# Kernel tuning notes

Hardware: AMD Instinct MI355X
Metric: run time of the kernel (lower is better)

## Reference

```python
import jax, jax.numpy as jnp
import numpy as np

B, L, HID, H, D = 1, 2048, 3072, 24, 128
MLP = 4 * HID
LH, LW = 32, 56      # latent mask grid -> LH*LW image tokens at the END of the sequence
LIP = 16             # IP-adapter image tokens
IP_SCALE = 0.6


def setup_inputs() -> dict:
    key = jax.random.key(0)
    k = jax.random.split(key, 10)
    # Flux rotary pe layout [1,1,L,D//2,2,2]: pe[...,0]=[cos,-sin], pe[...,1]=[sin,cos]
    pos = jnp.arange(L, dtype=jnp.float32)
    freqs = 1.0 / (10000.0 ** (jnp.arange(0, D, 2, dtype=jnp.float32) / D))
    ang = pos[:, None] * freqs[None, :]            # [L, D//2]
    cos, sin = jnp.cos(ang), jnp.sin(ang)
    pe = jnp.stack([jnp.stack([cos, -sin], -1), jnp.stack([sin, cos], -1)], -2)[None, None]
    return {
        "x": jax.random.normal(k[0], (B, L, HID), jnp.float32),
        "vec": jax.random.normal(k[1], (B, HID), jnp.float32),
        "pe": pe,
        "img_mask": jax.random.uniform(k[2], (B, LH, LW), jnp.float32),
        "image_emb": jax.random.normal(k[3], (B, LIP, HID), jnp.float32),
        "mod_w": jax.random.normal(k[4], (3 * HID, HID), jnp.float32) * 0.02,
        "mod_b": jnp.zeros((3 * HID,), jnp.float32),
        "lin1_w": jax.random.normal(k[5], (3 * HID + MLP, HID), jnp.float32) * 0.02,
        "lin1_b": jnp.zeros((3 * HID + MLP,), jnp.float32),
        "q_scale": jnp.ones((D,), jnp.float32),
        "k_scale": jnp.ones((D,), jnp.float32),
        "lin2_w": jax.random.normal(k[6], (HID, HID + MLP), jnp.float32) * 0.02,
        "lin2_b": jnp.zeros((HID,), jnp.float32),
        "ipk_w": jax.random.normal(k[7], (HID, HID), jnp.float32) * 0.02,
        "ipv_w": jax.random.normal(k[8], (HID, HID), jnp.float32) * 0.02,
    }


def _rms(x, scale, eps):
    # RMSNorm over last dim (QKNorm / norm_added_k)
    return x * jax.lax.rsqrt(jnp.mean(x * x, -1, keepdims=True) + eps) * scale


def _apply_rope(x, pe):
    # x: [B,H,L,D]; pe: [1,1,L,D//2,2,2]
    xr = x.reshape(x.shape[:-1] + (D // 2, 1, 2))
    out = pe[..., 0] * xr[..., 0] + pe[..., 1] * xr[..., 1]  # [B,H,L,D//2,2]
    return out.reshape(x.shape)


def _sdpa(q, k, v):
    # q:[B,H,Lq,D] k,v:[B,H,Lk,D] -> [B,Lq,H*D]
    s = jnp.einsum('bhqd,bhkd->bhqk', q, k) / jnp.sqrt(jnp.float32(D))
    o = jnp.einsum('bhqk,bhkd->bhqd', jax.nn.softmax(s, -1), v)
    return o.transpose(0, 2, 1, 3).reshape(q.shape[0], q.shape[2], H * D)


def reference(x, vec, pe, img_mask, image_emb, mod_w, mod_b, lin1_w, lin1_b,
              q_scale, k_scale, lin2_w, lin2_b, ipk_w, ipv_w):
    # modulation: SiLU(vec) -> Linear -> (shift, scale, gate), each [B,1,HID]
    mod = jax.nn.silu(vec) @ mod_w.T + mod_b
    shift, scale, gate = [m[:, None, :] for m in jnp.split(mod, 3, -1)]
    # pre_norm: LayerNorm, no affine, eps 1e-6 (biased variance, matches torch)
    ln = (x - jnp.mean(x, -1, keepdims=True)) * jax.lax.rsqrt(jnp.var(x, -1, keepdims=True) + 1e-6)
    x_mod = (1.0 + scale) * ln + shift
    # fused qkv + mlp projection
    h = x_mod @ lin1_w.T + lin1_b
    qkv, mlp = h[..., :3 * HID], h[..., 3 * HID:]
    q, k, v = qkv.reshape(B, L, 3, H, D).transpose(2, 0, 3, 1, 4)  # each [B,H,L,D]
    q = _rms(q, q_scale, 1e-6)
    k = _rms(k, k_scale, 1e-6)
    # rp_attention: RoPE then SDPA
    attn = _sdpa(_apply_rope(q, pe), _apply_rope(k, pe), v)       # [B,L,HID]
    # IP-adapter cross-attention: pre-rope q attends to projected image_emb
    ip_k = _rms((image_emb @ ipk_w.T).reshape(B, LIP, H, D).transpose(0, 2, 1, 3), 1.0, 1e-5)
    ip_v = (image_emb @ ipv_w.T).reshape(B, LIP, H, D).transpose(0, 2, 1, 3)
    ip_h = IP_SCALE * _sdpa(q, ip_k, ip_v)                        # [B,L,HID]
    # spatial mask applied to last LH*LW tokens, zeros elsewhere
    full_mask = jnp.concatenate(
        [jnp.zeros((B, L - LH * LW), ip_h.dtype), img_mask.reshape(B, LH * LW)], 1)
    attn = attn + ip_h * full_mask[..., None]
    out = jnp.concatenate([attn, jax.nn.gelu(mlp, approximate=True)], -1) @ lin2_w.T + lin2_b
    return x + gate * out
```

## Files before the change

kernel.cpp:

```cpp
#include <hip/hip_runtime.h>

#define HID 3072
#define LSEQ 2048
#define NH 24
#define HD 128
#define N1 21504
#define K2 15360

typedef unsigned short ushort_t;
typedef __attribute__((ext_vector_type(8))) short bf16x8;
typedef __attribute__((ext_vector_type(4))) float f32x4;

__device__ __forceinline__ unsigned short f2bf(float f) {
    union { float f; unsigned int u; } v; v.f = f;
    unsigned int u = v.u;
    u += 0x7fffu + ((u >> 16) & 1u);
    return (unsigned short)(u >> 16);
}
__device__ __forceinline__ float bf2f(unsigned short s) {
    union { unsigned int u; float f; } v; v.u = ((unsigned int)s) << 16;
    return v.f;
}
__device__ __forceinline__ float gelu_tanh(float x) {
    float u = 0.7978845608028654f * (x + 0.044715f * x * x * x);
    float t = 2.0f / (1.0f + __expf(-2.0f * u)) - 1.0f;
    return 0.5f * x * (1.0f + t);
}
__device__ __forceinline__ void gload_lds16(const ushort_t* g, ushort_t* l) {
    __builtin_amdgcn_global_load_lds((const __attribute__((address_space(1))) void*)g,
                                     (__attribute__((address_space(3))) void*)l, 16, 0, 0);
}

__global__ __launch_bounds__(256) void k_cvt2(const float* __restrict__ s1,
    ushort_t* __restrict__ d1, int n1, const float* __restrict__ s2,
    ushort_t* __restrict__ d2, int n2)
{
    int stride = gridDim.x * 256 * 8;
    int base = (blockIdx.x * 256 + threadIdx.x) * 8;
    for (int i = base; i < n1; i += stride) {
        float4 a = *reinterpret_cast<const float4*>(s1 + i);
        float4 b = *reinterpret_cast<const float4*>(s1 + i + 4);
        uint4 pk;
        pk.x = (unsigned)f2bf(a.x) | ((unsigned)f2bf(a.y) << 16);
        pk.y = (unsigned)f2bf(a.z) | ((unsigned)f2bf(a.w) << 16);
        pk.z = (unsigned)f2bf(b.x) | ((unsigned)f2bf(b.y) << 16);
        pk.w = (unsigned)f2bf(b.z) | ((unsigned)f2bf(b.w) << 16);
        *reinterpret_cast<uint4*>(d1 + i) = pk;
    }
    for (int i = base; i < n2; i += stride) {
        float4 a = *reinterpret_cast<const float4*>(s2 + i);
        float4 b = *reinterpret_cast<const float4*>(s2 + i + 4);
        uint4 pk;
        pk.x = (unsigned)f2bf(a.x) | ((unsigned)f2bf(a.y) << 16);
        pk.y = (unsigned)f2bf(a.z) | ((unsigned)f2bf(a.w) << 16);
        pk.z = (unsigned)f2bf(b.x) | ((unsigned)f2bf(b.y) << 16);
        pk.w = (unsigned)f2bf(b.z) | ((unsigned)f2bf(b.w) << 16);
        *reinterpret_cast<uint4*>(d2 + i) = pk;
    }
}

__global__ __launch_bounds__(256) void k_mod(const float* __restrict__ vec,
    const float* __restrict__ mw, const float* __restrict__ mb, float* __restrict__ mod) {
    __shared__ __align__(16) float sv[HID];
    int tid = threadIdx.x;
    for (int i = tid; i < HID; i += 256) {
        float v = vec[i];
        sv[i] = v / (1.0f + __expf(-v));
    }
    __syncthreads();
    int wave = tid >> 6, lane = tid & 63;
    int n = blockIdx.x * 4 + wave;
    const float* w = mw + (size_t)n * HID;
    float acc = 0.0f;
    for (int k = lane * 4; k < HID; k += 256) {
        float4 wv = *reinterpret_cast<const float4*>(w + k);
        float4 s  = *reinterpret_cast<const float4*>(sv + k);
        acc += wv.x * s.x + wv.y * s.y + wv.z * s.z + wv.w * s.w;
    }
    #pragma unroll
    for (int off = 1; off < 64; off <<= 1) acc += __shfl_xor(acc, off);
    if (lane == 0) mod[n] = acc + mb[n];
}

__global__ __launch_bounds__(256) void k_lnmod(const float* __restrict__ x,
    const float* __restrict__ mod, ushort_t* __restrict__ xmod) {
    int row = blockIdx.x, tid = threadIdx.x;
    const float4* xr = reinterpret_cast<const float4*>(x + (size_t)row * HID);
    float4 v[3];
    float s = 0.f, sq = 0.f;
    #pragma unroll
    for (int i = 0; i < 3; ++i) {
        v[i] = xr[tid + i * 256];
        s  += v[i].x + v[i].y + v[i].z + v[i].w;
        sq += v[i].x * v[i].x + v[i].y * v[i].y + v[i].z * v[i].z + v[i].w * v[i].w;
    }
    #pragma unroll
    for (int off = 1; off < 64; off <<= 1) { s += __shfl_xor(s, off); sq += __shfl_xor(sq, off); }
    __shared__ float rs[4], rq[4];
    int wave = tid >> 6, lane = tid & 63;
    if (lane == 0) { rs[wave] = s; rq[wave] = sq; }
    __syncthreads();
    s  = rs[0] + rs[1] + rs[2] + rs[3];
    sq = rq[0] + rq[1] + rq[2] + rq[3];
    float mean = s * (1.0f / HID);
    float var = sq * (1.0f / HID) - mean * mean;
    float rstd = rsqrtf(var + 1e-6f);
    ushort_t* orow = xmod + (size_t)row * HID;
    #pragma unroll
    for (int i = 0; i < 3; ++i) {
        int c = (tid + i * 256) * 4;
        float4 sc = *reinterpret_cast<const float4*>(mod + HID + c);
        float4 sh = *reinterpret_cast<const float4*>(mod + c);
        float o0 = (1.f + sc.x) * ((v[i].x - mean) * rstd) + sh.x;
        float o1 = (1.f + sc.y) * ((v[i].y - mean) * rstd) + sh.y;
        float o2 = (1.f + sc.z) * ((v[i].z - mean) * rstd) + sh.z;
        float o3 = (1.f + sc.w) * ((v[i].w - mean) * rstd) + sh.w;
        *reinterpret_cast<ushort4*>(orow + c) = make_ushort4(f2bf(o0), f2bf(o1), f2bf(o2), f2bf(o3));
    }
}

#define MFMA_CLUSTER(PH, AF)                                                          \
    do {                                                                              \
        __builtin_amdgcn_s_setprio(1);                                                \
        _Pragma("unroll") for (int i_ = 0; i_ < 2; ++i_)                              \
        _Pragma("unroll") for (int nj_ = 0; nj_ < 4; ++nj_)                           \
        _Pragma("unroll") for (int kh_ = 0; kh_ < 2; ++kh_)                           \
            acc[2 * (PH) + i_][nj_] = __builtin_amdgcn_mfma_f32_16x16x32_bf16(        \
                AF[i_][kh_], bfrag[nj_][kh_], acc[2 * (PH) + i_][nj_], 0, 0, 0);      \
        __builtin_amdgcn_s_setprio(0);                                                \
    } while (0)

__global__ __launch_bounds__(512) void k_gemm8(
    const ushort_t* __restrict__ A, const ushort_t* __restrict__ W,
    const float* __restrict__ bias,
    ushort_t* __restrict__ out_qkv, ushort_t* __restrict__ out_concat)
{
    extern __shared__ __align__(16) char smem_raw[];
    ushort_t* smem = (ushort_t*)smem_raw;
    const int Ks = HID;
    int tid = threadIdx.x;
    int wid = tid >> 6, l = tid & 63;
    int wm = wid >> 2, wn = wid & 3;
    int lr = l & 15, lg = l >> 4;

    int flat = blockIdx.y * 84 + blockIdx.x;
    int nf = (flat & 7) * 84 + (flat >> 3);
    int mt = nf & 7, nt = nf >> 3;
    int m0 = mt * 256, n0 = nt * 256;
    int NT = Ks >> 6;

    int lrow = l >> 3;
    int lc   = (l & 7) ^ lrow;
    int arow_st = wm * 128 + wn * 32 + lrow;
    int bhalf = wn >> 1, ridx = wm * 2 + (wn & 1);
    int brow_st = bhalf * 128 + ridx * 32 + lrow;
    const ushort_t* aSrc = A + (size_t)(m0 + arow_st) * Ks + lc * 8;
    const ushort_t* bSrc = W + (size_t)(n0 + brow_st) * Ks + lc * 8;
    int aDst = (wm * 128 + wn * 32) * 64;
    int bDst = (bhalf * 128 + ridx * 32) * 64;

    auto stageA = [&](int t, int buf, int c) {
        gload_lds16(aSrc + (size_t)c * 8 * Ks + (size_t)t * 64,
                    smem + buf * 16384 + aDst + c * 512);
    };
    auto stageB = [&](int t, int c) {
        gload_lds16(bSrc + (size_t)c * 8 * Ks + (size_t)t * 64,
                    smem + 49152 + (t & 1) * 16384 + bDst + c * 512);
    };
    auto readA = [&](int buf, int row, int ccc) {
        return *reinterpret_cast<const bf16x8*>(smem + buf * 16384 + row * 64 + ((ccc ^ (row & 7)) << 3));
    };
    auto readB = [&](int p, int row, int ccc) {
        return *reinterpret_cast<const bf16x8*>(smem + 49152 + p * 16384 + row * 64 + ((ccc ^ (row & 7)) << 3));
    };

    f32x4 acc[8][4] = {};

    #pragma unroll
    for (int c = 0; c < 4; ++c) stageA(0, 0, c);
    #pragma unroll
    for (int c = 0; c < 4; ++c) stageB(0, c);
    #pragma unroll
    for (int c = 0; c < 4; ++c) stageA(1, 1, c);
    #pragma unroll
    for (int c = 0; c < 4; ++c) stageB(1, c);
    asm volatile("s_waitcnt vmcnt(8)" ::: "memory");
    __builtin_amdgcn_s_barrier();

    int pA = 0, pA2 = 2;
    for (int t = 0; t < NT; ++t) {
        int pB = t & 1;
        bf16x8 bfrag[4][2], af0[2][2], af1[2][2], af2[2][2], af3[2][2];
        #pragma unroll
        for (int nj = 0; nj < 4; ++nj)
            #pragma unroll
            for (int kh = 0; kh < 2; ++kh)
                bfrag[nj][kh] = readB(pB, wn * 64 + nj * 16 + lr, kh * 4 + lg);
        #pragma unroll
        for (int i = 0; i < 2; ++i)
            #pragma unroll
            for (int kh = 0; kh < 2; ++kh)
                af0[i][kh] = readA(pA, wm * 128 + i * 16 + lr, kh * 4 + lg);
        if (t + 2 < NT) {
            stageA(t + 2, pA2, 0); stageA(t + 2, pA2, 1);
            stageA(t + 2, pA2, 2); stageA(t + 2, pA2, 3);
        }
        #pragma unroll
        for (int i = 0; i < 2; ++i)
            #pragma unroll
            for (int kh = 0; kh < 2; ++kh)
                af1[i][kh] = readA(pA, wm * 128 + (2 + i) * 16 + lr, kh * 4 + lg);
        MFMA_CLUSTER(0, af0);
        #pragma unroll
        for (int i = 0; i < 2; ++i)
            #pragma unroll
            for (int kh = 0; kh < 2; ++kh)
                af2[i][kh] = readA(pA, wm * 128 + (4 + i) * 16 + lr, kh * 4 + lg);
        MFMA_CLUSTER(1, af1);
        __builtin_amdgcn_s_barrier();
        if (t + 2 < NT) {
            stageB(t + 2, 0); stageB(t + 2, 1);
            stageB(t + 2, 2); stageB(t + 2, 3);
        }
        #pragma unroll
        for (int i = 0; i < 2; ++i)
            #pragma unroll
            for (int kh = 0; kh < 2; ++kh)
                af3[i][kh] = readA(pA, wm * 128 + (6 + i) * 16 + lr, kh * 4 + lg);
        MFMA_CLUSTER(2, af2);
        MFMA_CLUSTER(3, af3);
        if (t + 2 < NT)      asm volatile("s_waitcnt vmcnt(8)" ::: "memory");
        else if (t + 1 < NT) asm volatile("s_waitcnt vmcnt(0)" ::: "memory");
        __builtin_amdgcn_s_barrier();
        pA  = (pA  + 1 == 3) ? 0 : pA  + 1;
        pA2 = (pA2 + 1 == 3) ? 0 : pA2 + 1;
    }

    #pragma unroll
    for (int nj = 0; nj < 4; ++nj) {
        int col = n0 + wn * 64 + nj * 16 + lr;
        float b = bias[col];
        #pragma unroll
        for (int mi = 0; mi < 8; ++mi) {
            int rbase = m0 + wm * 128 + mi * 16 + lg * 4;
            #pragma unroll
            for (int r = 0; r < 4; ++r) {
                int mrow = rbase + r;
                float val = acc[mi][nj][r] + b;
                if (col < 3 * HID) {
                    out_qkv[(size_t)mrow * (3 * HID) + col] = f2bf(val);
                } else {
                    out_concat[(size_t)mrow * K2 + HID + (col - 3 * HID)] = f2bf(gelu_tanh(val));
                }
            }
        }
    }
}

#define MFMA_CL4(PH, AF)                                                              \
    do {                                                                              \
        __builtin_amdgcn_s_setprio(1);                                                \
        _Pragma("unroll") for (int nj_ = 0; nj_ < 4; ++nj_)                           \
        _Pragma("unroll") for (int kh_ = 0; kh_ < 2; ++kh_)                           \
            acc[(PH)][nj_] = __builtin_amdgcn_mfma_f32_16x16x32_bf16(                 \
                AF[kh_], bfrag[nj_][kh_], acc[(PH)][nj_], 0, 0, 0);                   \
        __builtin_amdgcn_s_setprio(0);                                                \
    } while (0)

__global__ __launch_bounds__(256) void k_gemm4(
    const ushort_t* __restrict__ A, const ushort_t* __restrict__ W,
    int klen, ushort_t* __restrict__ part)
{
    extern __shared__ __align__(16) char smem_raw[];
    ushort_t* smem = (ushort_t*)smem_raw;
    const int Ks = K2;
    int tid = threadIdx.x;
    int wave = tid >> 6, l = tid & 63;
    int wm = wave >> 1, wn = wave & 1;
    int lr = l & 15, lg = l >> 4;

    int flat = blockIdx.y * 24 + blockIdx.x;
    int nf = (flat & 7) * 48 + (flat >> 3);
    int mt = nf & 15, nt = nf >> 4;
    int m0 = mt * 128, n0 = nt * 128;
    int koff = blockIdx.z * klen;
    int NT = klen >> 6;

    int lrow = l >> 3;
    int lc   = (l & 7) ^ lrow;
    const ushort_t* aSrc = A + (size_t)(m0 + wave * 32 + lrow) * Ks + koff + lc * 8;
    const ushort_t* bSrc = W + (size_t)(n0 + wave * 32 + lrow) * Ks + koff + lc * 8;
    int dstBase = wave * 2048;

    auto stageA = [&](int t, int buf) {
        #pragma unroll
        for (int c = 0; c < 4; ++c)
            gload_lds16(aSrc + (size_t)c * 8 * Ks + (size_t)t * 64,
                        smem + buf * 8192 + dstBase + c * 512);
    };
    auto stageB = [&](int t) {
        #pragma unroll
        for (int c = 0; c < 4; ++c)
            gload_lds16(bSrc + (size_t)c * 8 * Ks + (size_t)t * 64,
                        smem + 24576 + (t & 1) * 8192 + dstBase + c * 512);
    };
    auto readA = [&](int buf, int row, int ccc) {
        return *reinterpret_cast<const bf16x8*>(smem + buf * 8192 + row * 64 + ((ccc ^ (row & 7)) << 3));
    };
    auto readB = [&](int p, int row, int ccc) {
        return *reinterpret_cast<const bf16x8*>(smem + 24576 + p * 8192 + row * 64 + ((ccc ^ (row & 7)) << 3));
    };

    f32x4 acc[4][4] = {};

    stageA(0, 0); stageB(0); stageA(1, 1); stageB(1);
    asm volatile("s_waitcnt vmcnt(8)" ::: "memory");
    __builtin_amdgcn_s_barrier();

    int pA = 0, pA2 = 2;
    for (int t = 0; t < NT; ++t) {
        int pB = t & 1;
        bf16x8 bfrag[4][2], af0[2], af1[2], af2[2], af3[2];
        #pragma unroll
        for (int nj = 0; nj < 4; ++nj)
            #pragma unroll
            for (int kh = 0; kh < 2; ++kh)
                bfrag[nj][kh] = readB(pB, wn * 64 + nj * 16 + lr, kh * 4 + lg);
        #pragma unroll
        for (int kh = 0; kh < 2; ++kh)
            af0[kh] = readA(pA, wm * 64 + lr, kh * 4 + lg);
        if (t + 2 < NT) stageA(t + 2, pA2);
        #pragma unroll
        for (int kh = 0; kh < 2; ++kh)
            af1[kh] = readA(pA, wm * 64 + 16 + lr, kh * 4 + lg);
        MFMA_CL4(0, af0);
        #pragma unroll
        for (int kh = 0; kh < 2; ++kh)
            af2[kh] = readA(pA, wm * 64 + 32 + lr, kh * 4 + lg);
        MFMA_CL4(1, af1);
        __builtin_amdgcn_s_barrier();
        if (t + 2 < NT) stageB(t + 2);
        #pragma unroll
        for (int kh = 0; kh < 2; ++kh)
            af3[kh] = readA(pA, wm * 64 + 48 + lr, kh * 4 + lg);
        MFMA_CL4(2, af2);
        MFMA_CL4(3, af3);
        if (t + 2 < NT)      asm volatile("s_waitcnt vmcnt(8)" ::: "memory");
        else if (t + 1 < NT) asm volatile("s_waitcnt vmcnt(0)" ::: "memory");
        __builtin_amdgcn_s_barrier();
        pA  = (pA  + 1 == 3) ? 0 : pA  + 1;
        pA2 = (pA2 + 1 == 3) ? 0 : pA2 + 1;
    }

    #pragma unroll
    for (int nj = 0; nj < 4; ++nj) {
        int col = n0 + wn * 64 + nj * 16 + lr;
        #pragma unroll
        for (int mi = 0; mi < 4; ++mi) {
            int rbase = m0 + wm * 64 + mi * 16 + lg * 4;
            #pragma unroll
            for (int r = 0; r < 4; ++r) {
                int mrow = rbase + r;
                part[(size_t)blockIdx.z * LSEQ * HID + (size_t)mrow * HID + col] = f2bf(acc[mi][nj][r]);
            }
        }
    }
}

__global__ __launch_bounds__(256) void k_red(const ushort_t* __restrict__ part,
    const float* __restrict__ bias, const float* __restrict__ xres,
    const float* __restrict__ mod, float* __restrict__ dout)
{
    size_t base = ((size_t)blockIdx.x * 256 + threadIdx.x) * 8;
    int col = (int)(base % HID);
    float s[8] = {0.f, 0.f, 0.f, 0.f, 0.f, 0.f, 0.f, 0.f};
    #pragma unroll
    for (int z = 0; z < 4; ++z) {
        uint4 pv = *reinterpret_cast<const uint4*>(part + (size_t)z * LSEQ * HID + base);
        unsigned w0 = pv.x, w1 = pv.y, w2 = pv.z, w3 = pv.w;
        s[0] += bf2f((ushort_t)(w0 & 0xffffu)); s[1] += bf2f((ushort_t)(w0 >> 16));
        s[2] += bf2f((ushort_t)(w1 & 0xffffu)); s[3] += bf2f((ushort_t)(w1 >> 16));
        s[4] += bf2f((ushort_t)(w2 & 0xffffu)); s[5] += bf2f((ushort_t)(w2 >> 16));
        s[6] += bf2f((ushort_t)(w3 & 0xffffu)); s[7] += bf2f((ushort_t)(w3 >> 16));
    }
    float4 bb0 = *reinterpret_cast<const float4*>(bias + col);
    float4 bb1 = *reinterpret_cast<const float4*>(bias + col + 4);
    float4 gg0 = *reinterpret_cast<const float4*>(mod + 2 * HID + col);
    float4 gg1 = *reinterpret_cast<const float4*>(mod + 2 * HID + col + 4);
    float4 xx0 = *reinterpret_cast<const float4*>(xres + base);
    float4 xx1 = *reinterpret_cast<const float4*>(xres + base + 4);
    float4 o0, o1;
    o0.x = xx0.x + gg0.x * (s[0] + bb0.x);
    o0.y = xx0.y + gg0.y * (s[1] + bb0.y);
    o0.z = xx0.z + gg0.z * (s[2] + bb0.z);
    o0.w = xx0.w + gg0.w * (s[3] + bb0.w);
    o1.x = xx1.x + gg1.x * (s[4] + bb1.x);
    o1.y = xx1.y + gg1.y * (s[5] + bb1.y);
    o1.z = xx1.z + gg1.z * (s[6] + bb1.z);
    o1.w = xx1.w + gg1.w * (s[7] + bb1.w);
    *reinterpret_cast<float4*>(dout + base) = o0;
    *reinterpret_cast<float4*>(dout + base + 4) = o1;
}

__global__ __launch_bounds__(256) void k_qkv(const ushort_t* __restrict__ qkv,
    const float* __restrict__ pe, const float* __restrict__ q_scale, const float* __restrict__ k_scale,
    ushort_t* __restrict__ q_rope, ushort_t* __restrict__ k_rope,
    ushort_t* __restrict__ q_rms, ushort_t* __restrict__ v_t)
{
    __shared__ ushort_t vtile[64][132];
    int h = blockIdx.y, l0 = blockIdx.x * 64;
    int wave = threadIdx.x >> 6, lane = threadIdx.x & 63;
    int d0 = lane * 2;
    float qs0 = q_scale[d0], qs1 = q_scale[d0 + 1];
    float ks0 = k_scale[d0], ks1 = k_scale[d0 + 1];
    for (int it = 0; it < 16; ++it) {
        int ll = it * 4 + wave;
        int l = l0 + ll;
        const ushort_t* base = qkv + (size_t)l * (3 * HID) + h * HD + d0;
        unsigned qw = *reinterpret_cast<const unsigned*>(base);
        unsigned kw = *reinterpret_cast<const unsigned*>(base + HID);
        unsigned vw = *reinterpret_cast<const unsigned*>(base + 2 * HID);
        float qx = bf2f((ushort_t)(qw & 0xffffu)), qy = bf2f((ushort_t)(qw >> 16));
        float kx = bf2f((ushort_t)(kw & 0xffffu)), ky = bf2f((ushort_t)(kw >> 16));
        float sq = qx * qx + qy * qy;
        float sk = kx * kx + ky * ky;
        #pragma unroll
        for (int off = 1; off < 64; off <<= 1) { sq += __shfl_xor(sq, off); sk += __shfl_xor(sk, off); }
        float rqv = rsqrtf(sq * (1.0f / HD) + 1e-6f);
        float rkv = rsqrtf(sk * (1.0f / HD) + 1e-6f);
        float qnx = qx * rqv * qs0, qny = qy * rqv * qs1;
        float knx = kx * rkv * ks0, kny = ky * rkv * ks1;
        float4 p = *reinterpret_cast<const float4*>(pe + ((size_t)l * 64 + lane) * 4);
        size_t off_hl = ((size_t)h * LSEQ + l) * HD + d0;
        *reinterpret_cast<unsigned*>(q_rms + off_hl) = (unsigned)f2bf(qnx) | ((unsigned)f2bf(qny) << 16);
        float qrx = p.x * qnx + p.y * qny, qry = p.z * qnx + p.w * qny;
        float krx = p.x * knx + p.y * kny, kry = p.z * knx + p.w * kny;
        *reinterpret_cast<unsigned*>(q_rope + off_hl) = (unsigned)f2bf(qrx) | ((unsigned)f2bf(qry) << 16);
        *reinterpret_cast<unsigned*>(k_rope + off_hl) = (unsigned)f2bf(krx) | ((unsigned)f2bf(kry) << 16);
        vtile[ll][d0] = (ushort_t)(vw & 0xffffu);
        vtile[ll][d0 + 1] = (ushort_t)(vw >> 16);
    }
    __syncthreads();
    int d = threadIdx.x >> 1, half = threadIdx.x & 1;
    ushort_t* dst = v_t + ((size_t)h * HD + d) * LSEQ + l0 + half * 32;
    #pragma unroll
    for (int g = 0; g < 4; ++g) {
        unsigned w0, w1, w2, w3;
        int lb = half * 32 + g * 8;
        w0 = (unsigned)vtile[lb + 0][d] | ((unsigned)vtile[lb + 1][d] << 16);
        w1 = (unsigned)vtile[lb + 2][d] | ((unsigned)vtile[lb + 3][d] << 16);
        w2 = (unsigned)vtile[lb + 4][d] | ((unsigned)vtile[lb + 5][d] << 16);
        w3 = (unsigned)vtile[lb + 6][d] | ((unsigned)vtile[lb + 7][d] << 16);
        reinterpret_cast<uint4*>(dst)[g] = make_uint4(w0, w1, w2, w3);
    }
}

__global__ __launch_bounds__(256) void k_ipgemv(const float* __restrict__ emb,
    const float* __restrict__ wk, const float* __restrict__ wv,
    float* __restrict__ ipk, float* __restrict__ ipv)
{
    int task = blockIdx.x * 4 + (threadIdx.x >> 6);
    int lane = threadIdx.x & 63;
    int which = task / HID;
    int n = task % HID;
    const float* w = (which ? wv : wk) + (size_t)n * HID;
    float acc[16];
    #pragma unroll
    for (int t = 0; t < 16; ++t) acc[t] = 0.f;
    for (int k = lane; k < HID; k += 64) {
        float wval = w[k];
        #pragma unroll
        for (int t = 0; t < 16; ++t) acc[t] += emb[t * HID + k] * wval;
    }
    #pragma unroll
    for (int off = 1; off < 64; off <<= 1) {
        #pragma unroll
        for (int t = 0; t < 16; ++t) acc[t] += __shfl_xor(acc[t], off);
    }
    if (lane == 0) {
        int hh = n >> 7, d = n & 127;
        float* dstp = which ? ipv : ipk;
        #pragma unroll
        for (int t = 0; t < 16; ++t) dstp[((size_t)hh * 16 + t) * HD + d] = acc[t];
    }
}

__global__ __launch_bounds__(256) void k_ipkrms(float* __restrict__ ipk) {
    int row = blockIdx.x * 4 + (threadIdx.x >> 6);
    int lane = threadIdx.x & 63;
    float2 v = *reinterpret_cast<const float2*>(ipk + (size_t)row * HD + lane * 2);
    float sq = v.x * v.x + v.y * v.y;
    #pragma unroll
    for (int off = 1; off < 64; off <<= 1) sq += __shfl_xor(sq, off);
    float r = rsqrtf(sq * (1.0f / HD) + 1e-5f);
    float2 o; o.x = v.x * r; o.y = v.y * r;
    *reinterpret_cast<float2*>(ipk + (size_t)row * HD + lane * 2) = o;
}

__global__ __launch_bounds__(256) void k_attn(const ushort_t* __restrict__ q_rope,
    const ushort_t* __restrict__ k_rope, const ushort_t* __restrict__ v_t,
    float* __restrict__ attnbuf)
{
    __shared__ __align__(16) ushort_t Ks[64 * 128];
    __shared__ __align__(16) ushort_t Vs[128 * 64];
    __shared__ __align__(16) ushort_t Ps[4 * 32 * 72];
    const float SC = 0.08838834764831845f;
    int flat = blockIdx.y * 16 + blockIdx.x;
    int nf = (flat & 7) * 48 + (flat >> 3);
    int h = nf >> 4, q0 = (nf & 15) << 7;
    int tid = threadIdx.x, wave = tid >> 6, lane = tid & 63;
    int lr = lane & 15, lg = lane >> 4;
    const ushort_t* Kb = k_rope + (size_t)h * LSEQ * HD;
    const ushort_t* Vb = v_t + (size_t)h * HD * LSEQ;
    bf16x8 qf[2][4];
    #pragma unroll
    for (int i = 0; i < 2; ++i) {
        #pragma unroll
        for (int ks = 0; ks < 4; ++ks) {
            int row = q0 + wave * 32 + i * 16 + lr;
            int d = ks * 32 + lg * 8;
            qf[i][ks] = *reinterpret_cast<const bf16x8*>(q_rope + ((size_t)h * LSEQ + row) * HD + d);
        }
    }
    f32x4 o[2][8] = {};
    float mrun[2][4], lrun[2][4];
    #pragma unroll
    for (int i = 0; i < 2; ++i)
        #pragma unroll
        for (int r = 0; r < 4; ++r) { mrun[i][r] = -1e30f; lrun[i][r] = 0.f; }

    uint4 kreg[4], vreg[4];
    auto loadKV = [&](int kt) {
        #pragma unroll
        for (int ii = 0; ii < 4; ++ii) {
            int c = tid + ii * 256;
            int krow = c >> 4, kc = c & 15;
            kreg[ii] = *reinterpret_cast<const uint4*>(Kb + (size_t)(kt + krow) * HD + kc * 8);
            int dr = c >> 3, vc = c & 7;
            vreg[ii] = *reinterpret_cast<const uint4*>(Vb + (size_t)dr * LSEQ + kt + vc * 8);
        }
    };
    loadKV(0);

    for (int kt = 0; kt < LSEQ; kt += 64) {
        #pragma unroll
        for (int ii = 0; ii < 4; ++ii) {
            int c = tid + ii * 256;
            int krow = c >> 4, kc = c & 15;
            *reinterpret_cast<uint4*>(reinterpret_cast<char*>(Ks) + krow * 256 + ((kc ^ (krow & 15)) << 4)) = kreg[ii];
            int dr = c >> 3, vc = c & 7;
            *reinterpret_cast<uint4*>(reinterpret_cast<char*>(Vs) + dr * 128 + ((vc ^ (dr & 7)) << 4)) = vreg[ii];
        }
        __syncthreads();
        if (kt + 64 < LSEQ) loadKV(kt + 64);
        f32x4 s[2][4] = {};
        __builtin_amdgcn_s_setprio(1);
        #pragma unroll
        for (int ks = 0; ks < 4; ++ks) {
            bf16x8 kf[4];
            #pragma unroll
            for (int j = 0; j < 4; ++j) {
                int krow = j * 16 + lr;
                int cc = ks * 4 + lg;
                kf[j] = *reinterpret_cast<const bf16x8*>(reinterpret_cast<char*>(Ks) + krow * 256 + ((cc ^ (krow & 15)) << 4));
            }
            #pragma unroll
            for (int i = 0; i < 2; ++i)
                #pragma unroll
                for (int j = 0; j < 4; ++j)
                    s[i][j] = __builtin_amdgcn_mfma_f32_16x16x32_bf16(qf[i][ks], kf[j], s[i][j], 0, 0, 0);
        }
        __builtin_amdgcn_s_setprio(0);
        float alpha[2][4];
        #pragma unroll
        for (int i = 0; i < 2; ++i) {
            #pragma unroll
            for (int r = 0; r < 4; ++r) {
                float v0 = s[i][0][r] * SC, v1 = s[i][1][r] * SC;
                float v2 = s[i][2][r] * SC, v3 = s[i][3][r] * SC;
                float mx = fmaxf(fmaxf(v0, v1), fmaxf(v2, v3));
                #pragma unroll
                for (int off = 1; off < 16; off <<= 1) mx = fmaxf(mx, __shfl_xor(mx, off));
                float mnew = fmaxf(mrun[i][r], mx);
                float al = __expf(mrun[i][r] - mnew);
                float p0 = __expf(v0 - mnew), p1 = __expf(v1 - mnew);
                float p2 = __expf(v2 - mnew), p3 = __expf(v3 - mnew);
                float rs2 = p0 + p1 + p2 + p3;
                #pragma unroll
                for (int off = 1; off < 16; off <<= 1) rs2 += __shfl_xor(rs2, off);
                lrun[i][r] = lrun[i][r] * al + rs2;
                mrun[i][r] = mnew;
                alpha[i][r] = al;
                s[i][0][r] = p0; s[i][1][r] = p1; s[i][2][r] = p2; s[i][3][r] = p3;
            }
        }
        #pragma unroll
        for (int i = 0; i < 2; ++i)
            #pragma unroll
            for (int j8 = 0; j8 < 8; ++j8)
                #pragma unroll
                for (int r = 0; r < 4; ++r) o[i][j8][r] *= alpha[i][r];
        #pragma unroll
        for (int i = 0; i < 2; ++i)
            #pragma unroll
            for (int j = 0; j < 4; ++j)
                #pragma unroll
                for (int r = 0; r < 4; ++r) {
                    int ql = i * 16 + lg * 4 + r;
                    int kp = j * 16 + lr;
                    Ps[wave * 2304 + ql * 72 + kp] = f2bf(s[i][j][r]);
                }
        __syncthreads();
        bf16x8 pa[2][2];
        #pragma unroll
        for (int i = 0; i < 2; ++i)
            #pragma unroll
            for (int ks2 = 0; ks2 < 2; ++ks2)
                pa[i][ks2] = *reinterpret_cast<const bf16x8*>(Ps + wave * 2304 + (i * 16 + lr) * 72 + ks2 * 32 + lg * 8);
        __builtin_amdgcn_s_setprio(1);
        #pragma unroll
        for (int j8 = 0; j8 < 8; ++j8) {
            int d = j8 * 16 + lr;
            #pragma unroll
            for (int ks2 = 0; ks2 < 2; ++ks2) {
                int cc = ks2 * 4 + lg;
                bf16x8 vf = *reinterpret_cast<const bf16x8*>(reinterpret_cast<char*>(Vs) + d * 128 + ((cc ^ (d & 7)) << 4));
                #pragma unroll
                for (int i = 0; i < 2; ++i)
                    o[i][j8] = __builtin_amdgcn_mfma_f32_16x16x32_bf16(pa[i][ks2], vf, o[i][j8], 0, 0, 0);
            }
        }
        __builtin_amdgcn_s_setprio(0);
        __syncthreads();
    }
    #pragma unroll
    for (int i = 0; i < 2; ++i) {
        #pragma unroll
        for (int r = 0; r < 4; ++r) {
            float inv = 1.0f / lrun[i][r];
            int mrow = q0 + wave * 32 + i * 16 + lg * 4 + r;
            float* orow = attnbuf + (size_t)mrow * HID + h * HD;
            #pragma unroll
            for (int j8 = 0; j8 < 8; ++j8)
                orow[j8 * 16 + lr] = o[i][j8][r] * inv;
        }
    }
}

__global__ __launch_bounds__(256) void k_ipattn(const ushort_t* __restrict__ q_rms,
    const float* __restrict__ ipk, const float* __restrict__ ipv,
    const float* __restrict__ attnbuf, const float* __restrict__ img_mask,
    ushort_t* __restrict__ concat)
{
    int task = blockIdx.x * 4 + (threadIdx.x >> 6);
    int lane = threadIdx.x & 63;
    int h = task >> 11;
    int l = task & 2047;
    int d0 = lane * 2;
    float2 a = *reinterpret_cast<const float2*>(attnbuf + (size_t)l * HID + h * HD + d0);
    if (l >= 256) {
        float mask = img_mask[l - 256];
        unsigned qv = *reinterpret_cast<const unsigned*>(q_rms + ((size_t)h * LSEQ + l) * HD + d0);
        float qx = bf2f((unsigned short)(qv & 0xffffu)), qy = bf2f((unsigned short)(qv >> 16));
        float s[16];
        const float* kb = ipk + (size_t)h * 16 * HD + d0;
        #pragma unroll
        for (int j = 0; j < 16; ++j) {
            float2 kk = *reinterpret_cast<const float2*>(kb + j * HD);
            float part = qx * kk.x + qy * kk.y;
            #pragma unroll
            for (int off = 1; off < 64; off <<= 1) part += __shfl_xor(part, off);
            s[j] = part * 0.08838834764831845f;
        }
        float mx = s[0];
        #pragma unroll
        for (int j = 1; j < 16; ++j) mx = fmaxf(mx, s[j]);
        float sum = 0.f;
        #pragma unroll
        for (int j = 0; j < 16; ++j) { s[j] = __expf(s[j] - mx); sum += s[j]; }
        float ox = 0.f, oy = 0.f;
        const float* vb = ipv + (size_t)h * 16 * HD + d0;
        #pragma unroll
        for (int j = 0; j < 16; ++j) {
            float2 vv = *reinterpret_cast<const float2*>(vb + j * HD);
            ox += s[j] * vv.x; oy += s[j] * vv.y;
        }
        float f = 0.6f * mask / sum;
        a.x += f * ox; a.y += f * oy;
    }
    *reinterpret_cast<unsigned*>(concat + (size_t)l * K2 + h * HD + d0) =
        (unsigned)f2bf(a.x) | ((unsigned)f2bf(a.y) << 16);
}

extern "C" void kernel_launch(void* const* d_in, const int* in_sizes, int n_in,
                              void* d_out, int out_size, void* d_ws, size_t ws_size,
                              hipStream_t stream)
{
    (void)in_sizes; (void)n_in; (void)out_size; (void)ws_size;
    const float* x         = (const float*)d_in[0];
    const float* vec       = (const float*)d_in[1];
    const float* pe        = (const float*)d_in[2];
    const float* img_mask  = (const float*)d_in[3];
    const float* image_emb = (const float*)d_in[4];
    const float* mod_w     = (const float*)d_in[5];
    const float* mod_b     = (const float*)d_in[6];
    const float* lin1_w    = (const float*)d_in[7];
    const float* lin1_b    = (const float*)d_in[8];
    const float* q_scale   = (const float*)d_in[9];
    const float* k_scale   = (const float*)d_in[10];
    const float* lin2_w    = (const float*)d_in[11];
    const float* lin2_b    = (const float*)d_in[12];
    const float* ipk_w     = (const float*)d_in[13];
    const float* ipv_w     = (const float*)d_in[14];
    float* dout = (float*)d_out;

    char* wp = (char*)d_ws;
    auto alloc = [&](size_t bytes) { char* p = wp; wp += (bytes + 255) & ~(size_t)255; return p; };
    float*    mod     = (float*)   alloc((size_t)9216 * 4);
    ushort_t* concat  = (ushort_t*)alloc((size_t)LSEQ * K2 * 2);
    ushort_t* lin2_bf = (ushort_t*)alloc((size_t)HID * K2 * 2);
    float*    ipk     = (float*)   alloc((size_t)NH * 16 * HD * 4);
    float*    ipv     = (float*)   alloc((size_t)NH * 16 * HD * 4);
    char* ubase = wp;
    ushort_t* lin1_bf = (ushort_t*)alloc((size_t)N1 * HID * 2);
    ushort_t* xmod    = (ushort_t*)alloc((size_t)LSEQ * HID * 2);
    ushort_t* qkv     = (ushort_t*)alloc((size_t)LSEQ * 3 * HID * 2);
    float*    attnbuf = (float*)   alloc((size_t)LSEQ * HID * 4);
    ushort_t* q_rope  = (ushort_t*)alloc((size_t)NH * LSEQ * HD * 2);
    ushort_t* k_rope  = (ushort_t*)alloc((size_t)NH * LSEQ * HD * 2);
    ushort_t* q_rms   = (ushort_t*)alloc((size_t)NH * LSEQ * HD * 2);
    ushort_t* v_t     = (ushort_t*)alloc((size_t)NH * HD * LSEQ * 2);
    ushort_t* partial = (ushort_t*)ubase;

    hipFuncSetAttribute((const void*)k_gemm8, hipFuncAttributeMaxDynamicSharedMemorySize, 163840);
    hipFuncSetAttribute((const void*)k_gemm4, hipFuncAttributeMaxDynamicSharedMemorySize, 81920);

    k_cvt2  <<<dim3(4096), dim3(256), 0, stream>>>(lin1_w, lin1_bf, N1 * HID,
                                                   lin2_w, lin2_bf, HID * K2);
    k_mod   <<<dim3(9216 / 4), dim3(256), 0, stream>>>(vec, mod_w, mod_b, mod);
    k_lnmod <<<dim3(LSEQ), dim3(256), 0, stream>>>(x, mod, xmod);
    k_gemm8 <<<dim3(84, 8), dim3(512), 163840, stream>>>(xmod, lin1_bf, lin1_b, qkv, concat);
    k_qkv   <<<dim3(32, NH), dim3(256), 0, stream>>>(qkv, pe, q_scale, k_scale,
                                                     q_rope, k_rope, q_rms, v_t);
    k_ipgemv<<<dim3(2 * HID / 4), dim3(256), 0, stream>>>(image_emb, ipk_w, ipv_w, ipk, ipv);
    k_ipkrms<<<dim3(NH * 16 / 4), dim3(256), 0, stream>>>(ipk);
    k_attn  <<<dim3(16, NH), dim3(256), 0, stream>>>(q_rope, k_rope, v_t, attnbuf);
    k_ipattn<<<dim3(NH * LSEQ / 4), dim3(256), 0, stream>>>(q_rms, ipk, ipv, attnbuf, img_mask, concat);
    k_gemm4 <<<dim3(24, 16, 4), dim3(256), 81920, stream>>>(concat, lin2_bf, 3840, partial);
    k_red   <<<dim3(LSEQ * HID / 2048), dim3(256), 0, stream>>>(partial, lin2_b, x, mod, dout);
}
```

Before: 1.132 ms.

## Shrink attention q-tile to 64 rows and drop K/V register prefetch

The flash-attention kernel now gives each block 64 query rows (16 per wave) instead of 128, doubling the grid to 768 blocks. The register double-buffered K/V prefetch and the swizzled block-order remap are removed, so K/V tiles are loaded straight into shared memory each iteration. The aim is more blocks and lower register pressure for better occupancy across the CUs. In exchange, each K/V tile is reused by half as many queries, so K/V traffic from global memory doubles and load latency is no longer hidden by prefetch.

```diff
diff --git a/kernel.cpp b/kernel.cpp
--- a/kernel.cpp
+++ b/kernel.cpp
@@ -503,57 +503,37 @@
 {
     __shared__ __align__(16) ushort_t Ks[64 * 128];
     __shared__ __align__(16) ushort_t Vs[128 * 64];
-    __shared__ __align__(16) ushort_t Ps[4 * 32 * 72];
+    __shared__ __align__(16) ushort_t Ps[4 * 16 * 72];
     const float SC = 0.08838834764831845f;
-    int flat = blockIdx.y * 16 + blockIdx.x;
-    int nf = (flat & 7) * 48 + (flat >> 3);
-    int h = nf >> 4, q0 = (nf & 15) << 7;
+    int h = blockIdx.y, q0 = blockIdx.x * 64;
     int tid = threadIdx.x, wave = tid >> 6, lane = tid & 63;
     int lr = lane & 15, lg = lane >> 4;
     const ushort_t* Kb = k_rope + (size_t)h * LSEQ * HD;
     const ushort_t* Vb = v_t + (size_t)h * HD * LSEQ;
-    bf16x8 qf[2][4];
-    #pragma unroll
-    for (int i = 0; i < 2; ++i) {
-        #pragma unroll
-        for (int ks = 0; ks < 4; ++ks) {
-            int row = q0 + wave * 32 + i * 16 + lr;
-            int d = ks * 32 + lg * 8;
-            qf[i][ks] = *reinterpret_cast<const bf16x8*>(q_rope + ((size_t)h * LSEQ + row) * HD + d);
-        }
-    }
-    f32x4 o[2][8] = {};
-    float mrun[2][4], lrun[2][4];
-    #pragma unroll
-    for (int i = 0; i < 2; ++i)
-        #pragma unroll
-        for (int r = 0; r < 4; ++r) { mrun[i][r] = -1e30f; lrun[i][r] = 0.f; }
-
-    uint4 kreg[4], vreg[4];
-    auto loadKV = [&](int kt) {
+    bf16x8 qf[4];
+    #pragma unroll
+    for (int ks = 0; ks < 4; ++ks) {
+        int row = q0 + wave * 16 + lr;
+        qf[ks] = *reinterpret_cast<const bf16x8*>(q_rope + ((size_t)h * LSEQ + row) * HD + ks * 32 + lg * 8);
+    }
+    f32x4 o[8] = {};
+    float mrun[4], lrun[4];
+    #pragma unroll
+    for (int r = 0; r < 4; ++r) { mrun[r] = -1e30f; lrun[r] = 0.f; }
+
+    for (int kt = 0; kt < LSEQ; kt += 64) {
         #pragma unroll
         for (int ii = 0; ii < 4; ++ii) {
             int c = tid + ii * 256;
             int krow = c >> 4, kc = c & 15;
-            kreg[ii] = *reinterpret_cast<const uint4*>(Kb + (size_t)(kt + krow) * HD + kc * 8);
+            uint4 va = *reinterpret_cast<const uint4*>(Kb + (size_t)(kt + krow) * HD + kc * 8);
+            *reinterpret_cast<uint4*>(reinterpret_cast<char*>(Ks) + krow * 256 + ((kc ^ (krow & 15)) << 4)) = va;
             int dr = c >> 3, vc = c & 7;
-            vreg[ii] = *reinterpret_cast<const uint4*>(Vb + (size_t)dr * LSEQ + kt + vc * 8);
-        }
-    };
-    loadKV(0);
-
-    for (int kt = 0; kt < LSEQ; kt += 64) {
-        #pragma unroll
-        for (int ii = 0; ii < 4; ++ii) {
-            int c = tid + ii * 256;
-            int krow = c >> 4, kc = c & 15;
-            *reinterpret_cast<uint4*>(reinterpret_cast<char*>(Ks) + krow * 256 + ((kc ^ (krow & 15)) << 4)) = kreg[ii];
-            int dr = c >> 3, vc = c & 7;
-            *reinterpret_cast<uint4*>(reinterpret_cast<char*>(Vs) + dr * 128 + ((vc ^ (dr & 7)) << 4)) = vreg[ii];
+            uint4 vb = *reinterpret_cast<const uint4*>(Vb + (size_t)dr * LSEQ + kt + vc * 8);
+            *reinterpret_cast<uint4*>(reinterpret_cast<char*>(Vs) + dr * 128 + ((vc ^ (dr & 7)) << 4)) = vb;
         }
         __syncthreads();
-        if (kt + 64 < LSEQ) loadKV(kt + 64);
-        f32x4 s[2][4] = {};
+        f32x4 s[4] = {};
         __builtin_amdgcn_s_setprio(1);
         #pragma unroll
         for (int ks = 0; ks < 4; ++ks) {
@@ -565,58 +545,46 @@
                 kf[j] = *reinterpret_cast<const bf16x8*>(reinterpret_cast<char*>(Ks) + krow * 256 + ((cc ^ (krow & 15)) << 4));
             }
             #pragma unroll
-            for (int i = 0; i < 2; ++i)
-                #pragma unroll
-                for (int j = 0; j < 4; ++j)
-                    s[i][j] = __builtin_amdgcn_mfma_f32_16x16x32_bf16(qf[i][ks], kf[j], s[i][j], 0, 0, 0);
+            for (int j = 0; j < 4; ++j)
+                s[j] = __builtin_amdgcn_mfma_f32_16x16x32_bf16(qf[ks], kf[j], s[j], 0, 0, 0);
         }
         __builtin_amdgcn_s_setprio(0);
-        float alpha[2][4];
-        #pragma unroll
-        for (int i = 0; i < 2; ++i) {
+        float alpha[4];
+        #pragma unroll
+        for (int r = 0; r < 4; ++r) {
+            float v0 = s[0][r] * SC, v1 = s[1][r] * SC;
+            float v2 = s[2][r] * SC, v3 = s[3][r] * SC;
+            float mx = fmaxf(fmaxf(v0, v1), fmaxf(v2, v3));
+            #pragma unroll
+            for (int off = 1; off < 16; off <<= 1) mx = fmaxf(mx, __shfl_xor(mx, off));
+            float mnew = fmaxf(mrun[r], mx);
+            float al = __expf(mrun[r] - mnew);
+            float p0 = __expf(v0 - mnew), p1 = __expf(v1 - mnew);
+            float p2 = __expf(v2 - mnew), p3 = __expf(v3 - mnew);
+            float rs2 = p0 + p1 + p2 + p3;
+            #pragma unroll
+            for (int off = 1; off < 16; off <<= 1) rs2 += __shfl_xor(rs2, off);
+            lrun[r] = lrun[r] * al + rs2;
+            mrun[r] = mnew;
+            alpha[r] = al;
+            s[0][r] = p0; s[1][r] = p1; s[2][r] = p2; s[3][r] = p3;
+        }
+        #pragma unroll
+        for (int j8 = 0; j8 < 8; ++j8)
+            #pragma unroll
+            for (int r = 0; r < 4; ++r) o[j8][r] *= alpha[r];
+        #pragma unroll
+        for (int j = 0; j < 4; ++j)
             #pragma unroll
             for (int r = 0; r < 4; ++r) {
-                float v0 = s[i][0][r] * SC, v1 = s[i][1][r] * SC;
-                float v2 = s[i][2][r] * SC, v3 = s[i][3][r] * SC;
-                float mx = fmaxf(fmaxf(v0, v1), fmaxf(v2, v3));
-                #pragma unroll
-                for (int off = 1; off < 16; off <<= 1) mx = fmaxf(mx, __shfl_xor(mx, off));
-                float mnew = fmaxf(mrun[i][r], mx);
-                float al = __expf(mrun[i][r] - mnew);
-                float p0 = __expf(v0 - mnew), p1 = __expf(v1 - mnew);
-                float p2 = __expf(v2 - mnew), p3 = __expf(v3 - mnew);
-                float rs2 = p0 + p1 + p2 + p3;
-                #pragma unroll
-                for (int off = 1; off < 16; off <<= 1) rs2 += __shfl_xor(rs2, off);
-                lrun[i][r] = lrun[i][r] * al + rs2;
-                mrun[i][r] = mnew;
-                alpha[i][r] = al;
-                s[i][0][r] = p0; s[i][1][r] = p1; s[i][2][r] = p2; s[i][3][r] = p3;
+                int ql = lg * 4 + r;
+                Ps[wave * 1152 + ql * 72 + j * 16 + lr] = f2bf(s[j][r]);
             }
-        }
-        #pragma unroll
-        for (int i = 0; i < 2; ++i)
-            #pragma unroll
-            for (int j8 = 0; j8 < 8; ++j8)
-                #pragma unroll
-                for (int r = 0; r < 4; ++r) o[i][j8][r] *= alpha[i][r];
-        #pragma unroll
-        for (int i = 0; i < 2; ++i)
-            #pragma unroll
-            for (int j = 0; j < 4; ++j)
-                #pragma unroll
-                for (int r = 0; r < 4; ++r) {
-                    int ql = i * 16 + lg * 4 + r;
-                    int kp = j * 16 + lr;
-                    Ps[wave * 2304 + ql * 72 + kp] = f2bf(s[i][j][r]);
-                }
         __syncthreads();
-        bf16x8 pa[2][2];
-        #pragma unroll
-        for (int i = 0; i < 2; ++i)
-            #pragma unroll
-            for (int ks2 = 0; ks2 < 2; ++ks2)
-                pa[i][ks2] = *reinterpret_cast<const bf16x8*>(Ps + wave * 2304 + (i * 16 + lr) * 72 + ks2 * 32 + lg * 8);
+        bf16x8 pa[2];
+        #pragma unroll
+        for (int ks2 = 0; ks2 < 2; ++ks2)
+            pa[ks2] = *reinterpret_cast<const bf16x8*>(Ps + wave * 1152 + lr * 72 + ks2 * 32 + lg * 8);
         __builtin_amdgcn_s_setprio(1);
         #pragma unroll
         for (int j8 = 0; j8 < 8; ++j8) {
@@ -625,25 +593,20 @@
             for (int ks2 = 0; ks2 < 2; ++ks2) {
                 int cc = ks2 * 4 + lg;
                 bf16x8 vf = *reinterpret_cast<const bf16x8*>(reinterpret_cast<char*>(Vs) + d * 128 + ((cc ^ (d & 7)) << 4));
-                #pragma unroll
-                for (int i = 0; i < 2; ++i)
-                    o[i][j8] = __builtin_amdgcn_mfma_f32_16x16x32_bf16(pa[i][ks2], vf, o[i][j8], 0, 0, 0);
+                o[j8] = __builtin_amdgcn_mfma_f32_16x16x32_bf16(pa[ks2], vf, o[j8], 0, 0, 0);
             }
         }
         __builtin_amdgcn_s_setprio(0);
         __syncthreads();
     }
     #pragma unroll
-    for (int i = 0; i < 2; ++i) {
-        #pragma unroll
-        for (int r = 0; r < 4; ++r) {
-            float inv = 1.0f / lrun[i][r];
-            int mrow = q0 + wave * 32 + i * 16 + lg * 4 + r;
-            float* orow = attnbuf + (size_t)mrow * HID + h * HD;
-            #pragma unroll
-            for (int j8 = 0; j8 < 8; ++j8)
-                orow[j8 * 16 + lr] = o[i][j8][r] * inv;
-        }
+    for (int r = 0; r < 4; ++r) {
+        float inv = 1.0f / lrun[r];
+        int mrow = q0 + wave * 16 + lg * 4 + r;
+        float* orow = attnbuf + (size_t)mrow * HID + h * HD;
+        #pragma unroll
+        for (int j8 = 0; j8 < 8; ++j8)
+            orow[j8 * 16 + lr] = o[j8][r] * inv;
     }
 }
 
@@ -744,7 +707,7 @@
                                                      q_rope, k_rope, q_rms, v_t);
     k_ipgemv<<<dim3(2 * HID / 4), dim3(256), 0, stream>>>(image_emb, ipk_w, ipv_w, ipk, ipv);
     k_ipkrms<<<dim3(NH * 16 / 4), dim3(256), 0, stream>>>(ipk);
-    k_attn  <<<dim3(16, NH), dim3(256), 0, stream>>>(q_rope, k_rope, v_t, attnbuf);
+    k_attn  <<<dim3(32, NH), dim3(256), 0, stream>>>(q_rope, k_rope, v_t, attnbuf);
     k_ipattn<<<dim3(NH * LSEQ / 4), dim3(256), 0, stream>>>(q_rms, ipk, ipv, attnbuf, img_mask, concat);
     k_gemm4 <<<dim3(24, 16, 4), dim3(256), 81920, stream>>>(concat, lin2_bf, 3840, partial);
     k_red   <<<dim3(LSEQ * HID / 2048), dim3(256), 0, stream>>>(partial, lin2_b, x, mod, dout);
```

New measurement: 950.2 us. -16.1%, faster.
